# Optimization experiments

Measured on AMD Instinct MI355X. Metric: run time of the kernel, lower is better.

Reference implementation:

```python
import jax, jax.numpy as jnp
import numpy as np

B, T, E, H, D = 1, 2048, 1024, 16, 64  # H*D == E required by module


def setup_inputs() -> dict:
    key = jax.random.key(0)
    ks = jax.random.split(key, 9)
    s_in = (2.0 / E) ** 0.5
    return {
        "x": jax.random.normal(ks[0], (B, T, E), jnp.float32),
        "wq": jax.random.normal(ks[1], (H * D, E), jnp.float32) * E ** -0.5,
        "wk": jax.random.normal(ks[2], (H * D, E), jnp.float32) * E ** -0.5,
        "wv": jax.random.normal(ks[3], (H * D, E), jnp.float32) * E ** -0.5,
        "wr": jax.random.normal(ks[4], (H, E, T), jnp.float32) * s_in,
        "wvr": jax.random.normal(ks[5], (H * D, E), jnp.float32) * E ** -0.5,
        "wj": jax.random.normal(ks[6], (E, E), jnp.float32) * E ** -0.5,
        "gate": jnp.zeros((H, 3), jnp.float32),
        "wo": jax.random.normal(ks[7], (E, H * D), jnp.float32) * E ** -0.5,
    }


def reference(x, wq, wk, wv, wr, wvr, wj, gate, wo):
    Bx, Tx, Ex = x.shape
    Hh = wr.shape[0]
    Dd = wq.shape[0] // Hh
    scale = 1.0 / Dd ** 0.5
    neg = -jnp.inf
    mask = jnp.triu(jnp.ones((Tx, Tx), bool), 1)  # True above diagonal

    def heads(w):  # (B,T,H*D) -> (B,H,T,D)
        return (x @ w.T).reshape(Bx, Tx, Hh, Dd).transpose(0, 2, 1, 3)

    # --- branch 1: standard causal QKV attention ---
    q, k, v = heads(wq), heads(wk), heads(wv)
    qkv_attn = jnp.einsum('bhqd,bhkd->bhqk', q, k) * scale
    qkv_attn = jnp.where(mask, neg, qkv_attn)
    qkv_out = jnp.einsum('bhqk,bhkd->bhqd', jax.nn.softmax(qkv_attn, axis=-1), v)

    # --- branch 2: RRPRAM learned per-position scores ---
    rv = heads(wvr)
    r = jnp.einsum('bte,het->bht', x, wr[:, :, :Tx])  # (B,H,T) key scores
    r_attn = jnp.where(mask, neg, (r * scale)[:, :, None, :])  # (B,H,T,T)
    rrp_out = jnp.einsum('bhqk,bhkd->bhqd', jax.nn.softmax(r_attn, axis=-1), rv)

    # --- branch 3: Janus self-resonance ---
    echo = x @ wj.T            # (B,T,E)
    echo_back = echo @ wj      # F.linear(echo, wj.weight.T)
    scores = (x * echo_back).sum(-1) / Ex ** 0.5  # (B,T)
    j_attn = jnp.where(mask, neg, scores[:, :, None] * scores[:, None, :])  # (B,T,T)
    jA = jax.nn.softmax(j_attn, axis=-1)
    j_val = echo.reshape(Bx, Tx, Hh, Dd).transpose(0, 2, 1, 3)
    jan_out = jnp.einsum('bqk,bhkd->bhqd', jA, j_val)

    # --- gated combine + output proj ---
    g = jax.nn.softmax(gate, axis=-1)  # (H,3)
    out = (g[:, 0][None, :, None, None] * qkv_out
           + g[:, 1][None, :, None, None] * rrp_out
           + g[:, 2][None, :, None, None] * jan_out)
    out = out.transpose(0, 2, 1, 3).reshape(Bx, Tx, Hh * Dd)
    return out @ wo.T
```

## Files before the change

kernel.cpp:

```cpp
#include <hip/hip_runtime.h>
#include <cstddef>
#include <cstdint>

#define TT 2048
#define EE 1024
#define HH 16
#define NSP 4

typedef unsigned short ushort;
typedef unsigned int uint;
typedef __attribute__((ext_vector_type(8))) short short8;
typedef __attribute__((ext_vector_type(8))) _Float16 half8;
typedef __attribute__((ext_vector_type(4))) float f32x4;
typedef __attribute__((ext_vector_type(4))) ushort ushort4v;

__device__ __forceinline__ ushort f2bf(float f) {
  uint u = __builtin_bit_cast(uint, f);
  u = (u + 0x7FFFu + ((u >> 16) & 1u)) >> 16;
  return (ushort)u;
}
__device__ __forceinline__ float bf2f(ushort h) {
  return __builtin_bit_cast(float, (uint)h << 16);
}
__device__ __forceinline__ ushort f2h(float f) {
  return __builtin_bit_cast(ushort, (_Float16)f);
}

__device__ __forceinline__ void async16(ushort* lds, const ushort* g) {
  __builtin_amdgcn_global_load_lds(
      reinterpret_cast<const __attribute__((address_space(1))) void*>(
          reinterpret_cast<uintptr_t>(g)),
      reinterpret_cast<__attribute__((address_space(3))) void*>(
          static_cast<unsigned int>(reinterpret_cast<uintptr_t>(lds))),
      16, 0, 0);
}

__global__ __launch_bounds__(256) void cvt_xt(
    const float* __restrict__ in, ushort* __restrict__ obf,
    ushort* __restrict__ oh, float* __restrict__ outT,
    float* __restrict__ snorm)
{
  __shared__ float tile[32][33];
  if (blockIdx.x == 0 && blockIdx.y == 0) {
    for (int i = threadIdx.x; i < TT; i += 256) snorm[i] = 0.f;
  }
  const int bn = blockIdx.x * 32;
  const int bm = blockIdx.y * 32;
  const int c4 = (threadIdx.x & 7) * 4;
  const int r  = threadIdx.x >> 3;
  const size_t off = (size_t)(bm + r) * EE + bn + c4;
  float4 v = *(const float4*)(in + off);
  tile[r][c4 + 0] = v.x; tile[r][c4 + 1] = v.y;
  tile[r][c4 + 2] = v.z; tile[r][c4 + 3] = v.w;
  ushort4v b, h;
  b.x = f2bf(v.x); b.y = f2bf(v.y); b.z = f2bf(v.z); b.w = f2bf(v.w);
  h.x = f2h(v.x);  h.y = f2h(v.y);  h.z = f2h(v.z);  h.w = f2h(v.w);
  *(ushort4v*)(obf + off) = b;
  *(ushort4v*)(oh + off) = h;
  __syncthreads();
  const int t4 = (threadIdx.x & 7) * 4;
  const int e  = threadIdx.x >> 3;
  float4 w;
  w.x = tile[t4 + 0][e]; w.y = tile[t4 + 1][e];
  w.z = tile[t4 + 2][e]; w.w = tile[t4 + 3][e];
  *(float4*)(outT + (size_t)(bn + e) * TT + bm + t4) = w;
}

__global__ __launch_bounds__(256) void cvt_w_k(
    const float* __restrict__ s0, const float* __restrict__ s1,
    const float* __restrict__ s2, const float* __restrict__ s3,
    const float* __restrict__ s4, const float* __restrict__ s5,
    ushort* __restrict__ d0, ushort* __restrict__ d1,
    ushort* __restrict__ d2, ushort* __restrict__ d3,
    ushort* __restrict__ d4, ushort* __restrict__ d5, int n) {
  const int which = blockIdx.y;
  const float* src; ushort* dst;
  switch (which) {
    case 0: src = s0; dst = d0; break;
    case 1: src = s1; dst = d1; break;
    case 2: src = s2; dst = d2; break;
    case 3: src = s3; dst = d3; break;
    case 4: src = s4; dst = d4; break;
    default: src = s5; dst = d5; break;
  }
  int i = (blockIdx.x * 256 + threadIdx.x) * 4;
  if (i >= n) return;
  float4 v = *(const float4*)(src + i);
  ushort4v o;
  if (which == 5) {
    o.x = f2h(v.x); o.y = f2h(v.y); o.z = f2h(v.z); o.w = f2h(v.w);
  } else {
    o.x = f2bf(v.x); o.y = f2bf(v.y); o.z = f2bf(v.z); o.w = f2bf(v.w);
  }
  *(ushort4v*)(dst + i) = o;
}

__global__ __launch_bounds__(256) void proj5(
    const ushort* __restrict__ Abf, const ushort* __restrict__ Ah,
    const ushort* __restrict__ B0, const ushort* __restrict__ B1,
    const ushort* __restrict__ B2, const ushort* __restrict__ B3,
    const ushort* __restrict__ B4,
    ushort* __restrict__ C0, ushort* __restrict__ C1,
    ushort* __restrict__ C2, ushort* __restrict__ C3,
    ushort* __restrict__ C4, float* __restrict__ snorm,
    int M, int N, int K)
{
  const ushort* A; const ushort* B; ushort* C; int om;
  switch (blockIdx.z) {
    case 0: A = Abf; B = B0; C = C0; om = 1; break;
    case 1: A = Abf; B = B1; C = C1; om = 1; break;
    case 2: A = Abf; B = B2; C = C2; om = 2; break;
    case 3: A = Abf; B = B3; C = C3; om = 1; break;
    default: A = Ah; B = B4; C = C4; om = 3; break;
  }
  const bool f16 = (blockIdx.z == 4);
  __shared__ __align__(16) ushort As[2][128 * 64];
  __shared__ __align__(16) ushort Bs[2][128 * 64];
  const int tid = threadIdx.x;
  const int m0 = blockIdx.y * 128, n0 = blockIdx.x * 128;
  const int w = tid >> 6, lane = tid & 63;
  const int wr = w >> 1, wc = w & 1;
  const int lr = lane & 15, lk = lane >> 4;
  const int srow = lane >> 3;
  const int scol = ((lane & 7) ^ srow) * 8;
  const ushort* AgL = A + (size_t)(m0 + w * 32 + srow) * K + scol;
  const ushort* BgL = B + (size_t)(n0 + w * 32 + srow) * K + scol;
  const int sbase = (w * 32) * 64;
  const int s0 = (lk ^ (lr & 7)) * 8;
  f32x4 acc[4][4] = {};
  const int NT = K >> 6;
#pragma unroll
  for (int c = 0; c < 4; ++c) {
    async16(&As[0][sbase + c * 8 * 64], AgL + (size_t)c * 8 * K);
    async16(&Bs[0][sbase + c * 8 * 64], BgL + (size_t)c * 8 * K);
  }
  __syncthreads();
  for (int kt = 0; kt < NT; ++kt) {
    const int cur = kt & 1;
    if (kt + 1 < NT) {
      const int kn = (kt + 1) << 6;
#pragma unroll
      for (int c = 0; c < 4; ++c) {
        async16(&As[cur ^ 1][sbase + c * 8 * 64], AgL + (size_t)c * 8 * K + kn);
        async16(&Bs[cur ^ 1][sbase + c * 8 * 64], BgL + (size_t)c * 8 * K + kn);
      }
    }
    short8 a0[4], a1[4], b0[4], b1[4];
#pragma unroll
    for (int i = 0; i < 4; ++i) {
      const ushort* p = &As[cur][(wr * 64 + i * 16 + lr) * 64];
      a0[i] = *(const short8*)(p + s0);
      a1[i] = *(const short8*)(p + (s0 ^ 32));
    }
#pragma unroll
    for (int j = 0; j < 4; ++j) {
      const ushort* p = &Bs[cur][(wc * 64 + j * 16 + lr) * 64];
      b0[j] = *(const short8*)(p + s0);
      b1[j] = *(const short8*)(p + (s0 ^ 32));
    }
    if (f16) {
#pragma unroll
      for (int i = 0; i < 4; ++i)
#pragma unroll
        for (int j = 0; j < 4; ++j) {
          acc[i][j] = __builtin_amdgcn_mfma_f32_16x16x32_f16(
              __builtin_bit_cast(half8, a0[i]), __builtin_bit_cast(half8, b0[j]),
              acc[i][j], 0, 0, 0);
          acc[i][j] = __builtin_amdgcn_mfma_f32_16x16x32_f16(
              __builtin_bit_cast(half8, a1[i]), __builtin_bit_cast(half8, b1[j]),
              acc[i][j], 0, 0, 0);
        }
    } else {
#pragma unroll
      for (int i = 0; i < 4; ++i)
#pragma unroll
        for (int j = 0; j < 4; ++j) {
          acc[i][j] = __builtin_amdgcn_mfma_f32_16x16x32_bf16(
              a0[i], b0[j], acc[i][j], 0, 0, 0);
          acc[i][j] = __builtin_amdgcn_mfma_f32_16x16x32_bf16(
              a1[i], b1[j], acc[i][j], 0, 0, 0);
        }
    }
    __syncthreads();
  }
#pragma unroll
  for (int i = 0; i < 4; ++i)
#pragma unroll
    for (int r = 0; r < 4; ++r) {
      int row = m0 + wr * 64 + i * 16 + lk * 4 + r;
#pragma unroll
      for (int j = 0; j < 4; ++j) {
        int col = n0 + wc * 64 + j * 16 + lr;
        ushort v = (om == 2) ? f2h(acc[i][j][r]) : f2bf(acc[i][j][r]);
        if (om == 1)
          C[((size_t)(col >> 6) * M + row) * 64 + (col & 63)] = v;
        else if (om == 2)
          C[(size_t)(col >> 6) * 64 * M + (size_t)(col & 63) * M + row] = v;
        else
          C[(size_t)col * M + row] = v;
      }
    }
  if (om == 3) {
#pragma unroll
    for (int i = 0; i < 4; ++i)
#pragma unroll
      for (int r = 0; r < 4; ++r) {
        float p = 0.f;
#pragma unroll
        for (int j = 0; j < 4; ++j) p += acc[i][j][r] * acc[i][j][r];
        p += __shfl_xor(p, 1); p += __shfl_xor(p, 2);
        p += __shfl_xor(p, 4); p += __shfl_xor(p, 8);
        if (lr == 0)
          atomicAdd(&snorm[m0 + wr * 64 + i * 16 + lk * 4 + r], p);
      }
  }
}

template<bool CZ>
__global__ __launch_bounds__(256) void gemm_mfma(
    const ushort* __restrict__ A, const ushort* __restrict__ B,
    float* __restrict__ Cp, int M, int N, int K)
{
  __shared__ __align__(16) ushort As[2][128 * 64];
  __shared__ __align__(16) ushort Bs[2][128 * 64];
  const int tid = threadIdx.x;
  const int m0 = blockIdx.y * 128, n0 = blockIdx.x * 128;
  const int w = tid >> 6, lane = tid & 63;
  const int wr = w >> 1, wc = w & 1;
  const int lr = lane & 15, lk = lane >> 4;
  const int srow = lane >> 3;
  const int scol = ((lane & 7) ^ srow) * 8;
  const ushort* AgL = A + (size_t)(m0 + w * 32 + srow) * K + scol;
  const ushort* BgL = B + (size_t)(n0 + w * 32 + srow) * K + scol;
  const int sbase = (w * 32) * 64;
  const int s0 = (lk ^ (lr & 7)) * 8;
  f32x4 acc[4][4] = {};
  const int Keff = CZ ? (K < m0 + 128 ? K : m0 + 128) : K;
  const int NT = Keff >> 6;
#pragma unroll
  for (int c = 0; c < 4; ++c) {
    async16(&As[0][sbase + c * 8 * 64], AgL + (size_t)c * 8 * K);
    async16(&Bs[0][sbase + c * 8 * 64], BgL + (size_t)c * 8 * K);
  }
  __syncthreads();
  for (int kt = 0; kt < NT; ++kt) {
    const int cur = kt & 1;
    if (kt + 1 < NT) {
      const int kn = (kt + 1) << 6;
#pragma unroll
      for (int c = 0; c < 4; ++c) {
        async16(&As[cur ^ 1][sbase + c * 8 * 64], AgL + (size_t)c * 8 * K + kn);
        async16(&Bs[cur ^ 1][sbase + c * 8 * 64], BgL + (size_t)c * 8 * K + kn);
      }
    }
    short8 a0[4], a1[4], b0[4], b1[4];
#pragma unroll
    for (int i = 0; i < 4; ++i) {
      const ushort* p = &As[cur][(wr * 64 + i * 16 + lr) * 64];
      a0[i] = *(const short8*)(p + s0);
      a1[i] = *(const short8*)(p + (s0 ^ 32));
    }
#pragma unroll
    for (int j = 0; j < 4; ++j) {
      const ushort* p = &Bs[cur][(wc * 64 + j * 16 + lr) * 64];
      b0[j] = *(const short8*)(p + s0);
      b1[j] = *(const short8*)(p + (s0 ^ 32));
    }
#pragma unroll
    for (int i = 0; i < 4; ++i)
#pragma unroll
      for (int j = 0; j < 4; ++j) {
        acc[i][j] = __builtin_amdgcn_mfma_f32_16x16x32_bf16(
            a0[i], b0[j], acc[i][j], 0, 0, 0);
        acc[i][j] = __builtin_amdgcn_mfma_f32_16x16x32_bf16(
            a1[i], b1[j], acc[i][j], 0, 0, 0);
      }
    __syncthreads();
  }
#pragma unroll
  for (int i = 0; i < 4; ++i)
#pragma unroll
    for (int r = 0; r < 4; ++r) {
      int row = m0 + wr * 64 + i * 16 + lk * 4 + r;
#pragma unroll
      for (int j = 0; j < 4; ++j) {
        int col = n0 + wc * 64 + j * 16 + lr;
        Cp[(size_t)row * N + col] = acc[i][j][r];
      }
    }
}

__global__ __launch_bounds__(64) void flash_mfma(
    const ushort* __restrict__ Qg, const ushort* __restrict__ Kg,
    const ushort* __restrict__ Vg, float* __restrict__ pbuf, int T, int nqt)
{
  const int bid = blockIdx.x;
  const int xcd = bid & 7;
  const int ii = bid >> 3;
  const int h = xcd * 2 + (ii & 1);
  const int sp = (ii >> 1) & 3;
  const int w  = (ii >> 3) & 3;
  const int qt = (nqt - 1) - (ii >> 5);
  const int q0 = qt * 64;
  const int nk = qt + 1;
  const int span = (nk + NSP - 1) >> 2;
  const int kb = sp * span;
  const int ke = (nk < kb + span) ? nk : (kb + span);
  const int lane = threadIdx.x & 63;
  const int lr = lane & 15, lk = lane >> 4;
  const ushort* Q = Qg + (size_t)h * T * 64;
  const ushort* K = Kg + (size_t)h * T * 64;
  const ushort* V = Vg + (size_t)h * 64 * T;
  __shared__ __align__(16) ushort Ps[16 * 72];
  const float CEXP = 0.18033688f;

  f32x4 o[4] = {};
  float ls[4] = {0.f, 0.f, 0.f, 0.f};

  if (kb < ke) {
    short8 qa0 = *(const short8*)(Q + (size_t)(q0 + w * 16 + lr) * 64 + lk * 8);
    short8 qa1 = *(const short8*)(Q + (size_t)(q0 + w * 16 + lr) * 64 + 32 + lk * 8);
    short8 kb0[4], kb1[4], vb0[4], vb1[4], vn0[4], vn1[4];
#pragma unroll
    for (int c = 0; c < 4; ++c) {
      const ushort* kp = K + (size_t)(kb * 64 + c * 16 + lr) * 64 + lk * 8;
      kb0[c] = *(const short8*)kp;
      kb1[c] = *(const short8*)(kp + 32);
      const ushort* vp = V + (size_t)(c * 16 + lr) * T + kb * 64 + lk * 8;
      vb0[c] = *(const short8*)vp;
      vb1[c] = *(const short8*)(vp + 32);
    }
    for (int kt = kb; kt < ke; ++kt) {
      const int k0 = kt * 64;
      f32x4 s[4];
      __builtin_amdgcn_s_setprio(1);
#pragma unroll
      for (int c = 0; c < 4; ++c) {
        f32x4 z = {};
        z = __builtin_amdgcn_mfma_f32_16x16x32_bf16(qa0, kb0[c], z, 0, 0, 0);
        z = __builtin_amdgcn_mfma_f32_16x16x32_bf16(qa1, kb1[c], z, 0, 0, 0);
        s[c] = z;
      }
      __builtin_amdgcn_s_setprio(0);
      if (kt + 1 < ke) {
#pragma unroll
        for (int c = 0; c < 4; ++c) {
          const ushort* kp = K + (size_t)(k0 + 64 + c * 16 + lr) * 64 + lk * 8;
          kb0[c] = *(const short8*)kp;
          kb1[c] = *(const short8*)(kp + 32);
          const ushort* vp = V + (size_t)(c * 16 + lr) * T + k0 + 64 + lk * 8;
          vn0[c] = *(const short8*)vp;
          vn1[c] = *(const short8*)(vp + 32);
        }
      }
      float pv[4][4];
#pragma unroll
      for (int c = 0; c < 4; ++c)
#pragma unroll
        for (int r = 0; r < 4; ++r)
          pv[c][r] = exp2f(s[c][r] * CEXP);
      if (kt == qt) {
        const int rowbase = q0 + w * 16 + lk * 4;
#pragma unroll
        for (int c = 0; c < 4; ++c) {
          const int col = k0 + c * 16 + lr;
#pragma unroll
          for (int r = 0; r < 4; ++r)
            if (col > rowbase + r) pv[c][r] = 0.f;
        }
      }
#pragma unroll
      for (int c = 0; c < 4; ++c)
#pragma unroll
        for (int r = 0; r < 4; ++r) {
          ls[r] += pv[c][r];
          Ps[(lk * 4 + r) * 72 + c * 16 + lr] = f2h(pv[c][r]);
        }
      short8 pa0 = *(const short8*)(&Ps[lr * 72 + lk * 8]);
      short8 pa1 = *(const short8*)(&Ps[lr * 72 + 32 + lk * 8]);
      __builtin_amdgcn_s_setprio(1);
#pragma unroll
      for (int c = 0; c < 4; ++c) {
        o[c] = __builtin_amdgcn_mfma_f32_16x16x32_f16(
            __builtin_bit_cast(half8, pa0), __builtin_bit_cast(half8, vb0[c]),
            o[c], 0, 0, 0);
        o[c] = __builtin_amdgcn_mfma_f32_16x16x32_f16(
            __builtin_bit_cast(half8, pa1), __builtin_bit_cast(half8, vb1[c]),
            o[c], 0, 0, 0);
      }
      __builtin_amdgcn_s_setprio(0);
      if (kt + 1 < ke) {
#pragma unroll
        for (int c = 0; c < 4; ++c) {
          vb0[c] = vn0[c];
          vb1[c] = vn1[c];
        }
      }
    }
#pragma unroll
    for (int r = 0; r < 4; ++r) {
      ls[r] += __shfl_xor(ls[r], 1);
      ls[r] += __shfl_xor(ls[r], 2);
      ls[r] += __shfl_xor(ls[r], 4);
      ls[r] += __shfl_xor(ls[r], 8);
    }
  }
  float* pb = pbuf + ((size_t)(h * nqt + qt) * NSP + sp) * 4160;
#pragma unroll
  for (int c = 0; c < 4; ++c)
#pragma unroll
    for (int r = 0; r < 4; ++r) {
      int row = w * 16 + lk * 4 + r;
      pb[(size_t)row * 64 + c * 16 + lr] = o[c][r];
    }
  if (lr == 0) {
#pragma unroll
    for (int r = 0; r < 4; ++r)
      pb[4096 + w * 16 + lk * 4 + r] = ls[r];
  }
}

__global__ __launch_bounds__(256) void flash_merge(
    const float* __restrict__ pbuf, ushort* __restrict__ O, int T, int nqt)
{
  const int b = blockIdx.x;
  const int h = b / nqt, qt = b - h * nqt;
  const float* p0 = pbuf + (size_t)b * NSP * 4160;
  const float* p1 = p0 + 4160;
  const float* p2 = p1 + 4160;
  const float* p3 = p2 + 4160;
  ushort* Oh = O + ((size_t)h * T + qt * 64) * 64;
  __shared__ float lsum[64];
  if (threadIdx.x < 64)
    lsum[threadIdx.x] = p0[4096 + threadIdx.x] + p1[4096 + threadIdx.x] +
                        p2[4096 + threadIdx.x] + p3[4096 + threadIdx.x];
  __syncthreads();
  for (int i = threadIdx.x; i < 4096; i += 256) {
    int r = i >> 6;
    Oh[i] = f2bf((p0[i] + p1[i] + p2[i] + p3[i]) / lsum[r]);
  }
}

__global__ __launch_bounds__(256) void rscore3(
    const float* __restrict__ xT, const float* __restrict__ wr,
    float* __restrict__ rpart, int T, int E)
{
  const int h = blockIdx.y;
  const int e0 = blockIdx.z * 64;
  const int t0 = (blockIdx.x * 256 + threadIdx.x) * 4;
  const float* wrh = wr + (size_t)h * E * T;
  float4 acc = {0.f, 0.f, 0.f, 0.f};
#pragma unroll 4
  for (int e = e0; e < e0 + 64; ++e) {
    float4 xv = *(const float4*)(xT + (size_t)e * T + t0);
    float4 wv = *(const float4*)(wrh + (size_t)e * T + t0);
    acc.x += xv.x * wv.x;
    acc.y += xv.y * wv.y;
    acc.z += xv.z * wv.z;
    acc.w += xv.w * wv.w;
  }
  *(float4*)(rpart + ((size_t)blockIdx.z * HH + h) * T + t0) = acc;
}

__global__ __launch_bounds__(256) void rsoftmax2(
    const float* __restrict__ rpart, float* __restrict__ w, int T)
{
  const int h = blockIdx.x;
  __shared__ float rs[TT];
  __shared__ float red[4];
  for (int t = threadIdx.x; t < T; t += 256) {
    float a = 0.f;
#pragma unroll
    for (int s = 0; s < 16; ++s) a += rpart[((size_t)s * HH + h) * T + t];
    rs[t] = a;
  }
  __syncthreads();
  float mx = -1e30f;
  for (int t = threadIdx.x; t < T; t += 256) mx = fmaxf(mx, rs[t]);
#pragma unroll
  for (int o = 32; o; o >>= 1) mx = fmaxf(mx, __shfl_xor(mx, o));
  if ((threadIdx.x & 63) == 0) red[threadIdx.x >> 6] = mx;
  __syncthreads();
  mx = fmaxf(fmaxf(red[0], red[1]), fmaxf(red[2], red[3]));
  float* wh = w + (size_t)h * T;
  for (int t = threadIdx.x; t < T; t += 256)
    wh[t] = __expf((rs[t] - mx) * 0.125f);
}

__global__ __launch_bounds__(64) void rrp_part(
    const float* __restrict__ wgt, const ushort* __restrict__ rv,
    float* __restrict__ segsum, int T)
{
  const int h = blockIdx.x, seg = blockIdx.y, d = threadIdx.x;
  const int segLen = T >> 5;
  const float* wh = wgt + (size_t)h * T;
  const ushort* rvh = rv + (size_t)h * T * 64;
  const int kbeg = seg * segLen, kend = kbeg + segLen;
  float num = 0.f, den = 0.f;
  for (int k = kbeg; k < kend; ++k) {
    float wk = wh[k];
    num += wk * bf2f(rvh[(size_t)k * 64 + d]);
    den += wk;
  }
  float* o = segsum + ((size_t)h * 32 + seg) * 65;
  o[d] = num;
  if (d == 0) o[64] = den;
}

__global__ __launch_bounds__(64) void rrp_scan2(
    const float* __restrict__ wgt, const ushort* __restrict__ rv,
    const float* __restrict__ segsum, ushort* __restrict__ out, int T)
{
  const int h = blockIdx.x, seg = blockIdx.y, d = threadIdx.x;
  const int segLen = T >> 5;
  const float* wh = wgt + (size_t)h * T;
  const ushort* rvh = rv + (size_t)h * T * 64;
  ushort* oh = out + (size_t)h * T * 64;
  float num = 0.f, den = 0.f;
  for (int s = 0; s < seg; ++s) {
    const float* p = segsum + ((size_t)h * 32 + s) * 65;
    num += p[d];
    den += p[64];
  }
  const int kbeg = seg * segLen, kend = kbeg + segLen;
  for (int k = kbeg; k < kend; ++k) {
    float wk = wh[k];
    num += wk * bf2f(rvh[(size_t)k * 64 + d]);
    den += wk;
    oh[(size_t)k * 64 + d] = f2bf(num / den);
  }
}

__global__ __launch_bounds__(256) void janus_w(
    const float* __restrict__ snorm, ushort* __restrict__ Wb,
    float* __restrict__ den, int T)
{
  const int q = blockIdx.x;
  const float sq = snorm[q] * 0.03125f;
  float mx = -1e30f;
  for (int k = threadIdx.x; k <= q; k += 256)
    mx = fmaxf(mx, sq * (snorm[k] * 0.03125f));
#pragma unroll
  for (int o = 32; o; o >>= 1) mx = fmaxf(mx, __shfl_xor(mx, o));
  __shared__ float red[4];
  if ((threadIdx.x & 63) == 0) red[threadIdx.x >> 6] = mx;
  __syncthreads();
  mx = fmaxf(fmaxf(red[0], red[1]), fmaxf(red[2], red[3]));
  float sum = 0.f;
  ushort* Wq = Wb + (size_t)q * T;
  for (int k = threadIdx.x; k < T; k += 256) {
    float wv = (k <= q) ? __expf(sq * (snorm[k] * 0.03125f) - mx) : 0.f;
    ushort wb = f2bf(wv);
    Wq[k] = wb;
    sum += bf2f(wb);
  }
#pragma unroll
  for (int o = 32; o; o >>= 1) sum += __shfl_xor(sum, o);
  __syncthreads();
  if ((threadIdx.x & 63) == 0) red[threadIdx.x >> 6] = sum;
  __syncthreads();
  if (threadIdx.x == 0) den[q] = red[0] + red[1] + red[2] + red[3];
}

__global__ __launch_bounds__(256) void combine_kernel(
    const ushort* __restrict__ a1, const ushort* __restrict__ a2,
    const float* __restrict__ jraw, const float* __restrict__ denj,
    const float* __restrict__ gate, ushort* __restrict__ comb, int T)
{
  const int idx = blockIdx.x * 256 + threadIdx.x;
  const int t = idx >> 10;
  const int c = idx & 1023;
  const int h = c >> 6;
  const int d = c & 63;
  float g0 = gate[h * 3 + 0], g1 = gate[h * 3 + 1], g2 = gate[h * 3 + 2];
  float mg = fmaxf(g0, fmaxf(g1, g2));
  float e0 = __expf(g0 - mg), e1 = __expf(g1 - mg), e2 = __expf(g2 - mg);
  float inv = 1.f / (e0 + e1 + e2);
  const size_t hd = ((size_t)h * T + t) * 64 + d;
  float v = (e0 * bf2f(a1[hd]) + e1 * bf2f(a2[hd]) + e2 * jraw[idx] / denj[t]) * inv;
  comb[idx] = f2bf(v);
}

extern "C" void kernel_launch(void* const* d_in, const int* in_sizes, int n_in,
                              void* d_out, int out_size, void* d_ws, size_t ws_size,
                              hipStream_t stream)
{
  (void)in_sizes; (void)n_in; (void)out_size; (void)ws_size;
  const float* x    = (const float*)d_in[0];
  const float* wq   = (const float*)d_in[1];
  const float* wk   = (const float*)d_in[2];
  const float* wv   = (const float*)d_in[3];
  const float* wr   = (const float*)d_in[4];
  const float* wvr  = (const float*)d_in[5];
  const float* wj   = (const float*)d_in[6];
  const float* gate = (const float*)d_in[7];
  const float* wo   = (const float*)d_in[8];
  float* out = (float*)d_out;

  const int T = TT, E = EE, H = HH;
  const int nqt = T / 64;
  const size_t TE = (size_t)T * E;
  const size_t EE2 = (size_t)E * E;
  const size_t TT2 = (size_t)T * T;

  ushort* u = (ushort*)d_ws;
  ushort* xbf   = u;
  ushort* xh    = xbf + TE;
  ushort* wqb   = xh + TE;
  ushort* wkb   = wqb + EE2;
  ushort* wvb   = wkb + EE2;
  ushort* wvrb  = wvb + EE2;
  ushort* wob   = wvrb + EE2;
  ushort* wjh   = wob + EE2;
  ushort* qhb   = wjh + EE2;
  ushort* khb   = qhb + TE;
  ushort* vtb   = khb + TE;
  ushort* rvhb  = vtb + TE;
  ushort* echoT = rvhb + TE;
  ushort* a1b   = echoT + TE;
  ushort* a2b   = a1b + TE;
  ushort* Wbf   = a2b + TE;
  ushort* combb = Wbf + TT2;
  float* jraw   = (float*)(combb + TE);
  float* wwb    = jraw + TE;
  float* snorm  = wwb + (size_t)H * T;
  float* denj   = snorm + T;
  float* rpart  = denj + T;
  float* segsum = rpart + (size_t)16 * H * T;
  float* xT     = segsum + (size_t)H * 32 * 65;
  float* pbuf   = xT + TE;

  dim3 blk(256);
  cvt_xt<<<dim3(E / 32, T / 32), blk, 0, stream>>>(x, xbf, xh, xT, snorm);
  cvt_w_k<<<dim3((int)(EE2 / 1024), 6), blk, 0, stream>>>(
      wq, wk, wv, wvr, wo, wj, wqb, wkb, wvb, wvrb, wob, wjh, (int)EE2);

  proj5<<<dim3(E / 128, T / 128, 5), blk, 0, stream>>>(
      xbf, xh, wqb, wkb, wvb, wvrb, wjh,
      qhb, khb, vtb, rvhb, echoT, snorm, T, E, E);

  rscore3<<<dim3(T / 1024, H, 16), blk, 0, stream>>>(xT, wr, rpart, T, E);
  rsoftmax2<<<H, blk, 0, stream>>>(rpart, wwb, T);

  flash_mfma<<<dim3(H * nqt * NSP * 4), dim3(64), 0, stream>>>(
      qhb, khb, vtb, pbuf, T, nqt);
  flash_merge<<<H * nqt, blk, 0, stream>>>(pbuf, a1b, T, nqt);

  rrp_part<<<dim3(H, 32), dim3(64), 0, stream>>>(wwb, rvhb, segsum, T);
  rrp_scan2<<<dim3(H, 32), dim3(64), 0, stream>>>(wwb, rvhb, segsum, a2b, T);

  janus_w<<<T, blk, 0, stream>>>(snorm, Wbf, denj, T);
  gemm_mfma<true><<<dim3(E / 128, T / 128), blk, 0, stream>>>(
      Wbf, echoT, jraw, T, E, T);

  combine_kernel<<<(int)(TE / 256), blk, 0, stream>>>(a1b, a2b, jraw, denj,
                                                      gate, combb, T);
  gemm_mfma<false><<<dim3(E / 128, T / 128), blk, 0, stream>>>(
      combb, wob, (float*)out, T, E, E);
}
```

Baseline: 458.5 us.

## Fuse flash merge into combine, halve KV split, restructure rscore over heads

Fuses the flash-attention partial merge into the gated combine kernel, which drops one launch and the bf16 round trip through an intermediate attention buffer. Cuts the flash KV split count from 4 to 2 and loads V inside the loop instead of double-buffering it, which lowers register pressure but gives less overlap and fewer blocks. Rewrites the r-score reduction so each thread covers all 16 heads for one position, reusing x loads across heads, and doubles the e-split to 32 partials. The merge+combine kernel writes comb with strided per-head accesses, which may be less coalesced than before.

```diff
diff --git a/kernel.cpp b/kernel.cpp
--- a/kernel.cpp
+++ b/kernel.cpp
@@ -5,7 +5,7 @@
 #define TT 2048
 #define EE 1024
 #define HH 16
-#define NSP 4
+#define NSP 2
 
 typedef unsigned short ushort;
 typedef unsigned int uint;
@@ -298,12 +298,12 @@
   const int xcd = bid & 7;
   const int ii = bid >> 3;
   const int h = xcd * 2 + (ii & 1);
-  const int sp = (ii >> 1) & 3;
-  const int w  = (ii >> 3) & 3;
-  const int qt = (nqt - 1) - (ii >> 5);
+  const int sp = (ii >> 1) & 1;
+  const int w  = (ii >> 2) & 3;
+  const int qt = (nqt - 1) - (ii >> 4);
   const int q0 = qt * 64;
   const int nk = qt + 1;
-  const int span = (nk + NSP - 1) >> 2;
+  const int span = (nk + 1) >> 1;
   const int kb = sp * span;
   const int ke = (nk < kb + span) ? nk : (kb + span);
   const int lane = threadIdx.x & 63;
@@ -320,18 +320,22 @@
   if (kb < ke) {
     short8 qa0 = *(const short8*)(Q + (size_t)(q0 + w * 16 + lr) * 64 + lk * 8);
     short8 qa1 = *(const short8*)(Q + (size_t)(q0 + w * 16 + lr) * 64 + 32 + lk * 8);
-    short8 kb0[4], kb1[4], vb0[4], vb1[4], vn0[4], vn1[4];
+    short8 kb0[4], kb1[4];
 #pragma unroll
     for (int c = 0; c < 4; ++c) {
       const ushort* kp = K + (size_t)(kb * 64 + c * 16 + lr) * 64 + lk * 8;
       kb0[c] = *(const short8*)kp;
       kb1[c] = *(const short8*)(kp + 32);
-      const ushort* vp = V + (size_t)(c * 16 + lr) * T + kb * 64 + lk * 8;
-      vb0[c] = *(const short8*)vp;
-      vb1[c] = *(const short8*)(vp + 32);
     }
     for (int kt = kb; kt < ke; ++kt) {
       const int k0 = kt * 64;
+      short8 vb0[4], vb1[4];
+#pragma unroll
+      for (int c = 0; c < 4; ++c) {
+        const ushort* vp = V + (size_t)(c * 16 + lr) * T + k0 + lk * 8;
+        vb0[c] = *(const short8*)vp;
+        vb1[c] = *(const short8*)(vp + 32);
+      }
       f32x4 s[4];
       __builtin_amdgcn_s_setprio(1);
 #pragma unroll
@@ -348,9 +352,6 @@
           const ushort* kp = K + (size_t)(k0 + 64 + c * 16 + lr) * 64 + lk * 8;
           kb0[c] = *(const short8*)kp;
           kb1[c] = *(const short8*)(kp + 32);
-          const ushort* vp = V + (size_t)(c * 16 + lr) * T + k0 + 64 + lk * 8;
-          vn0[c] = *(const short8*)vp;
-          vn1[c] = *(const short8*)(vp + 32);
         }
       }
       float pv[4][4];
@@ -389,13 +390,6 @@
             o[c], 0, 0, 0);
       }
       __builtin_amdgcn_s_setprio(0);
-      if (kt + 1 < ke) {
-#pragma unroll
-        for (int c = 0; c < 4; ++c) {
-          vb0[c] = vn0[c];
-          vb1[c] = vn1[c];
-        }
-      }
     }
 #pragma unroll
     for (int r = 0; r < 4; ++r) {
@@ -420,46 +414,53 @@
   }
 }
 
-__global__ __launch_bounds__(256) void flash_merge(
-    const float* __restrict__ pbuf, ushort* __restrict__ O, int T, int nqt)
+__global__ __launch_bounds__(256) void merge_combine(
+    const float* __restrict__ pbuf, const ushort* __restrict__ a2,
+    const float* __restrict__ jraw, const float* __restrict__ denj,
+    const float* __restrict__ gate, ushort* __restrict__ comb, int T, int nqt)
 {
   const int b = blockIdx.x;
   const int h = b / nqt, qt = b - h * nqt;
   const float* p0 = pbuf + (size_t)b * NSP * 4160;
   const float* p1 = p0 + 4160;
-  const float* p2 = p1 + 4160;
-  const float* p3 = p2 + 4160;
-  ushort* Oh = O + ((size_t)h * T + qt * 64) * 64;
   __shared__ float lsum[64];
   if (threadIdx.x < 64)
-    lsum[threadIdx.x] = p0[4096 + threadIdx.x] + p1[4096 + threadIdx.x] +
-                        p2[4096 + threadIdx.x] + p3[4096 + threadIdx.x];
+    lsum[threadIdx.x] = p0[4096 + threadIdx.x] + p1[4096 + threadIdx.x];
+  float g0 = gate[h * 3 + 0], g1 = gate[h * 3 + 1], g2 = gate[h * 3 + 2];
+  float mg = fmaxf(g0, fmaxf(g1, g2));
+  float e0 = __expf(g0 - mg), e1 = __expf(g1 - mg), e2 = __expf(g2 - mg);
+  float inv = 1.f / (e0 + e1 + e2);
   __syncthreads();
   for (int i = threadIdx.x; i < 4096; i += 256) {
-    int r = i >> 6;
-    Oh[i] = f2bf((p0[i] + p1[i] + p2[i] + p3[i]) / lsum[r]);
-  }
-}
-
-__global__ __launch_bounds__(256) void rscore3(
+    const int r = i >> 6, d = i & 63;
+    const int t = qt * 64 + r;
+    const float o1 = (p0[i] + p1[i]) / lsum[r];
+    const size_t hd = ((size_t)h * T + t) * 64 + d;
+    const float v =
+        (e0 * o1 + e1 * bf2f(a2[hd]) +
+         e2 * jraw[(size_t)t * EE + h * 64 + d] / denj[t]) * inv;
+    comb[(size_t)t * EE + h * 64 + d] = f2bf(v);
+  }
+}
+
+__global__ __launch_bounds__(256) void rscore4(
     const float* __restrict__ xT, const float* __restrict__ wr,
     float* __restrict__ rpart, int T, int E)
 {
-  const int h = blockIdx.y;
-  const int e0 = blockIdx.z * 64;
-  const int t0 = (blockIdx.x * 256 + threadIdx.x) * 4;
-  const float* wrh = wr + (size_t)h * E * T;
-  float4 acc = {0.f, 0.f, 0.f, 0.f};
+  const int t = blockIdx.x * 256 + threadIdx.x;
+  const int e0 = blockIdx.y * 32;
+  float acc[HH] = {};
 #pragma unroll 4
-  for (int e = e0; e < e0 + 64; ++e) {
-    float4 xv = *(const float4*)(xT + (size_t)e * T + t0);
-    float4 wv = *(const float4*)(wrh + (size_t)e * T + t0);
-    acc.x += xv.x * wv.x;
-    acc.y += xv.y * wv.y;
-    acc.z += xv.z * wv.z;
-    acc.w += xv.w * wv.w;
-  }
-  *(float4*)(rpart + ((size_t)blockIdx.z * HH + h) * T + t0) = acc;
+  for (int e = e0; e < e0 + 32; ++e) {
+    const float xv = xT[(size_t)e * T + t];
+    const float* wp = wr + (size_t)e * T + t;
+#pragma unroll
+    for (int h = 0; h < HH; ++h)
+      acc[h] += xv * wp[(size_t)h * E * T];
+  }
+#pragma unroll
+  for (int h = 0; h < HH; ++h)
+    rpart[((size_t)blockIdx.y * HH + h) * T + t] = acc[h];
 }
 
 __global__ __launch_bounds__(256) void rsoftmax2(
@@ -471,7 +472,7 @@
   for (int t = threadIdx.x; t < T; t += 256) {
     float a = 0.f;
 #pragma unroll
-    for (int s = 0; s < 16; ++s) a += rpart[((size_t)s * HH + h) * T + t];
+    for (int s = 0; s < 32; ++s) a += rpart[((size_t)s * HH + h) * T + t];
     rs[t] = a;
   }
   __syncthreads();
@@ -560,25 +561,6 @@
   if ((threadIdx.x & 63) == 0) red[threadIdx.x >> 6] = sum;
   __syncthreads();
   if (threadIdx.x == 0) den[q] = red[0] + red[1] + red[2] + red[3];
-}
-
-__global__ __launch_bounds__(256) void combine_kernel(
-    const ushort* __restrict__ a1, const ushort* __restrict__ a2,
-    const float* __restrict__ jraw, const float* __restrict__ denj,
-    const float* __restrict__ gate, ushort* __restrict__ comb, int T)
-{
-  const int idx = blockIdx.x * 256 + threadIdx.x;
-  const int t = idx >> 10;
-  const int c = idx & 1023;
-  const int h = c >> 6;
-  const int d = c & 63;
-  float g0 = gate[h * 3 + 0], g1 = gate[h * 3 + 1], g2 = gate[h * 3 + 2];
-  float mg = fmaxf(g0, fmaxf(g1, g2));
-  float e0 = __expf(g0 - mg), e1 = __expf(g1 - mg), e2 = __expf(g2 - mg);
-  float inv = 1.f / (e0 + e1 + e2);
-  const size_t hd = ((size_t)h * T + t) * 64 + d;
-  float v = (e0 * bf2f(a1[hd]) + e1 * bf2f(a2[hd]) + e2 * jraw[idx] / denj[t]) * inv;
-  comb[idx] = f2bf(v);
 }
 
 extern "C" void kernel_launch(void* const* d_in, const int* in_sizes, int n_in,
@@ -617,8 +599,7 @@
   ushort* vtb   = khb + TE;
   ushort* rvhb  = vtb + TE;
   ushort* echoT = rvhb + TE;
-  ushort* a1b   = echoT + TE;
-  ushort* a2b   = a1b + TE;
+  ushort* a2b   = echoT + TE;
   ushort* Wbf   = a2b + TE;
   ushort* combb = Wbf + TT2;
   float* jraw   = (float*)(combb + TE);
@@ -626,7 +607,7 @@
   float* snorm  = wwb + (size_t)H * T;
   float* denj   = snorm + T;
   float* rpart  = denj + T;
-  float* segsum = rpart + (size_t)16 * H * T;
+  float* segsum = rpart + (size_t)32 * H * T;
   float* xT     = segsum + (size_t)H * 32 * 65;
   float* pbuf   = xT + TE;
 
@@ -639,12 +620,11 @@
       xbf, xh, wqb, wkb, wvb, wvrb, wjh,
       qhb, khb, vtb, rvhb, echoT, snorm, T, E, E);
 
-  rscore3<<<dim3(T / 1024, H, 16), blk, 0, stream>>>(xT, wr, rpart, T, E);
+  rscore4<<<dim3(T / 256, E / 32), blk, 0, stream>>>(xT, wr, rpart, T, E);
   rsoftmax2<<<H, blk, 0, stream>>>(rpart, wwb, T);
 
   flash_mfma<<<dim3(H * nqt * NSP * 4), dim3(64), 0, stream>>>(
       qhb, khb, vtb, pbuf, T, nqt);
-  flash_merge<<<H * nqt, blk, 0, stream>>>(pbuf, a1b, T, nqt);
 
   rrp_part<<<dim3(H, 32), dim3(64), 0, stream>>>(wwb, rvhb, segsum, T);
   rrp_scan2<<<dim3(H, 32), dim3(64), 0, stream>>>(wwb, rvhb, segsum, a2b, T);
@@ -653,8 +633,8 @@
   gemm_mfma<true><<<dim3(E / 128, T / 128), blk, 0, stream>>>(
       Wbf, echoT, jraw, T, E, T);
 
-  combine_kernel<<<(int)(TE / 256), blk, 0, stream>>>(a1b, a2b, jraw, denj,
-                                                      gate, combb, T);
+  merge_combine<<<H * nqt, blk, 0, stream>>>(pbuf, a2b, jraw, denj, gate,
+                                             combb, T, nqt);
   gemm_mfma<false><<<dim3(E / 128, T / 128), blk, 0, stream>>>(
       combb, wob, (float*)out, T, E, E);
 }
```

Result: slower. 565.0 us (+23.2%).
